# Kernel tuning notes

Hardware: AMD Instinct MI355X
Metric: run time of the kernel (lower is better)

The kernel has to match this reference:

```python
import jax, jax.numpy as jnp
import numpy as np

N = 8192      # nodes
D_IN = 128    # input features
D_H = 48      # GAT hidden (hardcoded in module)
D_OUT = 32    # control output dim
NEG_INF = -9e15  # matches torch code's -9000000000000000.0


def setup_inputs() -> dict:
    key = jax.random.key(0)
    ks = jax.random.split(key, 12)
    s = 0.05
    return {
        "x": jax.random.normal(ks[0], (N, D_IN), jnp.float32),
        "adj": jax.random.randint(ks[1], (N, N), 0, 2, jnp.int32),
        "W_gat": jax.random.normal(ks[2], (D_H, D_IN), jnp.float32) * s,
        "a": jax.random.normal(ks[3], (1, D_H), jnp.float32) * s,
        "gamma": jnp.ones((D_H,), jnp.float32),
        "beta": jnp.zeros((D_H,), jnp.float32),
        "W1": jax.random.normal(ks[4], (256, D_H), jnp.float32) * s,
        "b1": jnp.zeros((256,), jnp.float32),
        "W2": jax.random.normal(ks[5], (128, 256), jnp.float32) * s,
        "b2": jnp.zeros((128,), jnp.float32),
        "W3": jax.random.normal(ks[6], (D_OUT, 128), jnp.float32) * s,
        "b3": jnp.zeros((D_OUT,), jnp.float32),
    }


def reference(x, adj, W_gat, a, gamma, beta, W1, b1, W2, b2, W3, b3):
    # --- LightweightGATLayer ---
    Wh = x @ W_gat.T                      # [N, D_H]
    s = Wh @ a.T                          # [N, 1] additive attention scores
    e = s + s.T                           # [N, N]
    e = jnp.where(e > 0, e, 0.2 * e)      # LeakyReLU(0.2)
    e = jnp.where(adj > 0, e, NEG_INF)    # mask non-edges
    attn = jax.nn.softmax(e, axis=1)      # row softmax; dropout is identity in eval
    h_prime = attn @ Wh                   # [N, D_H]
    # LayerNorm over last dim, eps=1e-5
    mu = jnp.mean(h_prime, axis=-1, keepdims=True)
    var = jnp.var(h_prime, axis=-1, keepdims=True)
    h = (h_prime - mu) * jax.lax.rsqrt(var + 1e-5) * gamma + beta
    # --- BiACT MLP head: 48 -> 256 -> 128 -> D_OUT ---
    h = jax.nn.relu(h @ W1.T + b1)
    h = jax.nn.relu(h @ W2.T + b2)
    return h @ W3.T + b3                  # [N, D_OUT]
```

## Files before the change

kernel.cpp:

```cpp
#include <hip/hip_runtime.h>

#define N 8192
#define DIN 128
#define DH 48
#define MT 128
#define KC 64
#define PSTR 72
#define NSPLIT 16
#define JSPAN (N / NSPLIT)
#define NCHUNK (JSPAN / KC)
#define HSTR 49
#define RB 32

typedef _Float16 half8 __attribute__((ext_vector_type(8)));
typedef float f32x4 __attribute__((ext_vector_type(4)));

__global__ __launch_bounds__(256) void k_zero(float* __restrict__ hacc) {
    int i = blockIdx.x * 256 + threadIdx.x;
    if (i < N * HSTR) hacc[i] = 0.f;
}

__global__ __launch_bounds__(256) void k_wh(const float* __restrict__ x,
                                            const float* __restrict__ Wg,
                                            float* __restrict__ Wh) {
    __shared__ float wT[DIN * DH];
    int t = threadIdx.x;
    for (int e = t; e < DIN * DH; e += 256) {
        int c = e / DIN, k = e % DIN;
        wT[k * DH + c] = Wg[e];
    }
    __syncthreads();
    int o = blockIdx.x * 256 + t;
    int r = o / DH, c = o % DH;
    const float4* xr = (const float4*)(x + (size_t)r * DIN);
    float acc = 0.f;
    #pragma unroll 8
    for (int k4 = 0; k4 < DIN / 4; ++k4) {
        float4 xv = xr[k4];
        int kb = k4 * 4;
        acc += xv.x * wT[(kb + 0) * DH + c];
        acc += xv.y * wT[(kb + 1) * DH + c];
        acc += xv.z * wT[(kb + 2) * DH + c];
        acc += xv.w * wT[(kb + 3) * DH + c];
    }
    Wh[o] = acc;
}

__global__ __launch_bounds__(256) void k_s(const float* __restrict__ Wh,
                                           const float* __restrict__ a,
                                           float* __restrict__ s) {
    int r = blockIdx.x * 256 + threadIdx.x;
    const float4* wr = (const float4*)(Wh + (size_t)r * DH);
    const float4* av = (const float4*)a;
    float acc = 0.f;
    #pragma unroll
    for (int k4 = 0; k4 < DH / 4; ++k4) {
        float4 w = wr[k4]; float4 aa = av[k4];
        acc += w.x * aa.x + w.y * aa.y + w.z * aa.z + w.w * aa.w;
    }
    s[r] = acc;
}

__global__ __launch_bounds__(256) void k_tr(const float* __restrict__ Wh,
                                            _Float16* __restrict__ WhT) {
    __shared__ _Float16 tile[DH][72];
    int t = threadIdx.x;
    int r0 = blockIdx.x * 64;
    for (int e = t; e < 64 * DH; e += 256) {
        int r = e / DH, c = e % DH;
        tile[c][r] = (_Float16)Wh[(size_t)(r0 + r) * DH + c];
    }
    __syncthreads();
    for (int u = t; u < DH * 8; u += 256) {
        int c = u >> 3, g = u & 7;
        *(half8*)&WhT[(size_t)c * N + r0 + g * 8] = *(const half8*)&tile[c][g * 8];
    }
}

__global__ __launch_bounds__(256, 4) void k_gat(const int* __restrict__ adj,
                                                const _Float16* __restrict__ WhT,
                                                const float* __restrict__ s,
                                                float* __restrict__ hacc) {
    __shared__ _Float16 pS[MT][PSTR];
    __shared__ float sRow[MT];
    int t = threadIdx.x;
    int tile = blockIdx.x & 63;
    int split = blockIdx.x >> 6;
    int i0 = tile * MT;
    int jbase = split * JSPAN;

    if (t < MT) sRow[t] = s[i0 + t];

    int lane = t & 63, w = t >> 6;
    int ln16 = lane & 15, kq = lane >> 4;
    int jp = t & 31, rg = t >> 5;

    half8 bc;
    {
        _Float16 v = (ln16 == 0) ? (_Float16)1.0f : (_Float16)0.0f;
        #pragma unroll
        for (int i = 0; i < 8; ++i) bc[i] = v;
    }

    f32x4 acc[2][4];
    #pragma unroll
    for (int m = 0; m < 2; ++m)
        #pragma unroll
        for (int n = 0; n < 4; ++n) acc[m][n] = (f32x4){0.f, 0.f, 0.f, 0.f};

    __syncthreads();

    for (int chunk = 0; chunk < NCHUNK; ++chunk) {
        int j0 = jbase + chunk * KC;
        int2 av[16];
        {
            const int* abase = adj + (size_t)(i0 + rg * 16) * N + j0 + 2 * jp;
            #pragma unroll
            for (int it = 0; it < 16; ++it)
                av[it] = *(const int2*)(abase + (size_t)it * N);
        }
        half8 bfr[2][3];
        #pragma unroll
        for (int kt = 0; kt < 2; ++kt)
            #pragma unroll
            for (int nt = 0; nt < 3; ++nt)
                bfr[kt][nt] = *(const half8*)&WhT[(size_t)(nt * 16 + ln16) * N
                                                  + j0 + kt * 32 + kq * 8];
        {
            float2 sj = *(const float2*)(s + j0 + 2 * jp);
            #pragma unroll
            for (int it = 0; it < 16; ++it) {
                int r = rg * 16 + it;
                float e0 = sRow[r] + sj.x;
                float e1 = sRow[r] + sj.y;
                e0 = fmaxf(e0, 0.2f * e0);
                e1 = fmaxf(e1, 0.2f * e1);
                float p0 = av[it].x ? __expf(e0) : 0.f;
                float p1 = av[it].y ? __expf(e1) : 0.f;
                union { _Float16 h[2]; unsigned u; } pk;
                pk.h[0] = (_Float16)p0;
                pk.h[1] = (_Float16)p1;
                *(unsigned*)&pS[r][2 * jp] = pk.u;
            }
        }
        __syncthreads();
        {
            int m0 = w * 32;
            #pragma unroll
            for (int kt = 0; kt < 2; ++kt) {
                int kk = kt * 32 + kq * 8;
                #pragma unroll
                for (int mtl = 0; mtl < 2; ++mtl) {
                    half8 a = *(const half8*)&pS[m0 + mtl * 16 + ln16][kk];
                    acc[mtl][0] = __builtin_amdgcn_mfma_f32_16x16x32_f16(a, bfr[kt][0], acc[mtl][0], 0, 0, 0);
                    acc[mtl][1] = __builtin_amdgcn_mfma_f32_16x16x32_f16(a, bfr[kt][1], acc[mtl][1], 0, 0, 0);
                    acc[mtl][2] = __builtin_amdgcn_mfma_f32_16x16x32_f16(a, bfr[kt][2], acc[mtl][2], 0, 0, 0);
                    acc[mtl][3] = __builtin_amdgcn_mfma_f32_16x16x32_f16(a, bc,         acc[mtl][3], 0, 0, 0);
                }
            }
        }
        __syncthreads();
    }
    #pragma unroll
    for (int mtl = 0; mtl < 2; ++mtl) {
        int rbase = i0 + w * 32 + mtl * 16 + kq * 4;
        #pragma unroll
        for (int nt = 0; nt < 4; ++nt) {
            int col = nt * 16 + ln16;
            if (nt == 3 && ln16 != 0) continue;
            #pragma unroll
            for (int reg = 0; reg < 4; ++reg)
                atomicAdd(&hacc[(size_t)(rbase + reg) * HSTR + col], acc[mtl][nt][reg]);
        }
    }
}

__global__ __launch_bounds__(256) void k_mlp(const float* __restrict__ hacc,
                                             const float* __restrict__ gamma,
                                             const float* __restrict__ beta,
                                             const float* __restrict__ W1, const float* __restrict__ b1,
                                             const float* __restrict__ W2, const float* __restrict__ b2,
                                             const float* __restrict__ W3, const float* __restrict__ b3,
                                             float* __restrict__ out) {
    __shared__ float hs[RB * HSTR];
    __shared__ float hN[RB * DH];
    __shared__ float h1[RB * 256];
    __shared__ float h2[RB * 128];
    int t = threadIdx.x;
    int r0 = blockIdx.x * RB;

    for (int e = t; e < RB * HSTR; e += 256)
        hs[e] = hacc[(size_t)r0 * HSTR + e];
    __syncthreads();

    if (t < RB) {
        float invl = 1.f / hs[t * HSTR + 48];
        float sum = 0.f;
        for (int d = 0; d < DH; ++d) sum += hs[t * HSTR + d];
        float mean = sum * invl * (1.f / DH);
        float var = 0.f;
        for (int d = 0; d < DH; ++d) {
            float dv = hs[t * HSTR + d] * invl - mean;
            var += dv * dv;
        }
        var *= (1.f / DH);
        float rs = rsqrtf(var + 1e-5f);
        for (int d = 0; d < DH; ++d) {
            float hv = (hs[t * HSTR + d] * invl - mean) * rs;
            hN[t * DH + d] = hv * gamma[d] + beta[d];
        }
    }
    __syncthreads();

    {
        int c0 = (t & 127) * 2, c1 = c0 + 1;
        int rbeg = (t >> 7) * 16;
        float4 wa[12], wb[12];
        const float4* wr0 = (const float4*)(W1 + c0 * DH);
        const float4* wr1 = (const float4*)(W1 + c1 * DH);
        #pragma unroll
        for (int k4 = 0; k4 < 12; ++k4) { wa[k4] = wr0[k4]; wb[k4] = wr1[k4]; }
        float ba = b1[c0], bb = b1[c1];
        for (int r = rbeg; r < rbeg + 16; ++r) {
            const float4* hv4 = (const float4*)&hN[r * DH];
            float a0 = ba, a1 = bb;
            #pragma unroll
            for (int k4 = 0; k4 < 12; ++k4) {
                float4 hv = hv4[k4];
                a0 += hv.x * wa[k4].x + hv.y * wa[k4].y + hv.z * wa[k4].z + hv.w * wa[k4].w;
                a1 += hv.x * wb[k4].x + hv.y * wb[k4].y + hv.z * wb[k4].z + hv.w * wb[k4].w;
            }
            h1[r * 256 + c0] = fmaxf(a0, 0.f);
            h1[r * 256 + c1] = fmaxf(a1, 0.f);
        }
    }
    __syncthreads();

    {
        int c4 = (t & 31) * 4;
        int rr0 = (t >> 5) * 4;
        float a[4][4];
        #pragma unroll
        for (int rr = 0; rr < 4; ++rr)
            #pragma unroll
            for (int cc = 0; cc < 4; ++cc) a[rr][cc] = 0.f;
        for (int k4 = 0; k4 < 64; ++k4) {
            float4 h[4], wv[4];
            #pragma unroll
            for (int rr = 0; rr < 4; ++rr)
                h[rr] = *(const float4*)&h1[(rr0 + rr) * 256 + 4 * k4];
            #pragma unroll
            for (int cc = 0; cc < 4; ++cc)
                wv[cc] = *(const float4*)&W2[(size_t)(c4 + cc) * 256 + 4 * k4];
            #pragma unroll
            for (int rr = 0; rr < 4; ++rr)
                #pragma unroll
                for (int cc = 0; cc < 4; ++cc)
                    a[rr][cc] += h[rr].x * wv[cc].x + h[rr].y * wv[cc].y
                               + h[rr].z * wv[cc].z + h[rr].w * wv[cc].w;
        }
        #pragma unroll
        for (int rr = 0; rr < 4; ++rr)
            #pragma unroll
            for (int cc = 0; cc < 4; ++cc)
                h2[(rr0 + rr) * 128 + c4 + cc] = fmaxf(a[rr][cc] + b2[c4 + cc], 0.f);
    }
    __syncthreads();

    {
        int c = t & 31;
        int rr0 = (t >> 5) * 4;
        float a[4];
        float bias = b3[c];
        #pragma unroll
        for (int rr = 0; rr < 4; ++rr) a[rr] = bias;
        const float4* wrow = (const float4*)(W3 + c * 128);
        for (int k4 = 0; k4 < 32; ++k4) {
            float4 wv = wrow[k4];
            #pragma unroll
            for (int rr = 0; rr < 4; ++rr) {
                float4 hv = *(const float4*)&h2[(rr0 + rr) * 128 + 4 * k4];
                a[rr] += wv.x * hv.x + wv.y * hv.y + wv.z * hv.z + wv.w * hv.w;
            }
        }
        #pragma unroll
        for (int rr = 0; rr < 4; ++rr)
            out[(size_t)(r0 + rr0 + rr) * 32 + c] = a[rr];
    }
}

extern "C" void kernel_launch(void* const* d_in, const int* in_sizes, int n_in,
                              void* d_out, int out_size, void* d_ws, size_t ws_size,
                              hipStream_t stream) {
    const float* x     = (const float*)d_in[0];
    const int*   adj   = (const int*)d_in[1];
    const float* Wg    = (const float*)d_in[2];
    const float* a     = (const float*)d_in[3];
    const float* gamma = (const float*)d_in[4];
    const float* beta  = (const float*)d_in[5];
    const float* W1    = (const float*)d_in[6];
    const float* b1    = (const float*)d_in[7];
    const float* W2    = (const float*)d_in[8];
    const float* b2    = (const float*)d_in[9];
    const float* W3    = (const float*)d_in[10];
    const float* b3    = (const float*)d_in[11];
    float* out = (float*)d_out;

    float* ws = (float*)d_ws;
    float*     Wh   = ws;
    float*     s    = ws + (size_t)N * DH;
    _Float16*  WhT  = (_Float16*)(ws + (size_t)N * DH + N);
    float*     hacc = ws + (size_t)N * DH + N + (size_t)N * DH / 2;

    k_zero<<<(N * HSTR + 255) / 256, 256, 0, stream>>>(hacc);
    k_wh<<<N * DH / 256, 256, 0, stream>>>(x, Wg, Wh);
    k_s<<<N / 256, 256, 0, stream>>>(Wh, a, s);
    k_tr<<<N / 64, 256, 0, stream>>>(Wh, WhT);
    k_gat<<<64 * NSPLIT, 256, 0, stream>>>(adj, WhT, s, hacc);
    k_mlp<<<N / RB, 256, 0, stream>>>(hacc, gamma, beta, W1, b1, W2, b2, W3, b3, out);
}
```

Measured before the change: 497.6 us.

## Double-buffer GAT chunks with register prefetch and replace atomics with split partial sums

The GAT kernel now prefetches the next chunk's adjacency values into registers and stages the transposed Wh tile through double-buffered shared memory. This is meant to overlap global loads with the exp and MFMA work and to drop one barrier per chunk. The atomicAdd reduction into a zeroed accumulator is replaced by per-split partial stores, which the MLP kernel sums; that removes the zero kernel and the atomic contention. In exchange it uses more LDS and registers (launch bounds lowered to 3 waves) and adds a 16-way reduction read of a larger workspace.

```diff
diff --git a/kernel.cpp b/kernel.cpp
--- a/kernel.cpp
+++ b/kernel.cpp
@@ -9,16 +9,12 @@
 #define NSPLIT 16
 #define JSPAN (N / NSPLIT)
 #define NCHUNK (JSPAN / KC)
+#define ACC_STRIDE 64
 #define HSTR 49
 #define RB 32
 
 typedef _Float16 half8 __attribute__((ext_vector_type(8)));
 typedef float f32x4 __attribute__((ext_vector_type(4)));
-
-__global__ __launch_bounds__(256) void k_zero(float* __restrict__ hacc) {
-    int i = blockIdx.x * 256 + threadIdx.x;
-    if (i < N * HSTR) hacc[i] = 0.f;
-}
 
 __global__ __launch_bounds__(256) void k_wh(const float* __restrict__ x,
                                             const float* __restrict__ Wg,
@@ -77,11 +73,12 @@
     }
 }
 
-__global__ __launch_bounds__(256, 4) void k_gat(const int* __restrict__ adj,
+__global__ __launch_bounds__(256, 3) void k_gat(const int* __restrict__ adj,
                                                 const _Float16* __restrict__ WhT,
                                                 const float* __restrict__ s,
-                                                float* __restrict__ hacc) {
-    __shared__ _Float16 pS[MT][PSTR];
+                                                float* __restrict__ accWs) {
+    __shared__ _Float16 pS[2][MT][PSTR];
+    __shared__ _Float16 wS[2][DH][PSTR];
     __shared__ float sRow[MT];
     int t = threadIdx.x;
     int tile = blockIdx.x & 63;
@@ -108,24 +105,39 @@
         #pragma unroll
         for (int n = 0; n < 4; ++n) acc[m][n] = (f32x4){0.f, 0.f, 0.f, 0.f};
 
-    __syncthreads();
-
+    const int* arow = adj + (size_t)(i0 + rg * 16) * N + 2 * jp;
+
+    int2 av[16];
+    #pragma unroll
+    for (int it = 0; it < 16; ++it)
+        av[it] = *(const int2*)(arow + (size_t)it * N + jbase);
+    {
+        int u0 = t;
+        int row = u0 >> 3, s8 = u0 & 3 ;
+        s8 = u0 & 7;
+        if (u0 < 384) {  }
+        half8 v0 = *(const half8*)&WhT[(size_t)row * N + jbase + s8 * 8];
+        *(half8*)&wS[0][row][s8 * 8] = v0;
+        if (t < 128) {
+            int u1 = 256 + t;
+            int row1 = u1 >> 3, s81 = u1 & 7;
+            half8 v1 = *(const half8*)&WhT[(size_t)row1 * N + jbase + s81 * 8];
+            *(half8*)&wS[0][row1][s81 * 8] = v1;
+        }
+    }
+    __syncthreads();
+
+    int buf = 0;
     for (int chunk = 0; chunk < NCHUNK; ++chunk) {
         int j0 = jbase + chunk * KC;
-        int2 av[16];
-        {
-            const int* abase = adj + (size_t)(i0 + rg * 16) * N + j0 + 2 * jp;
+        bool more = (chunk + 1 < NCHUNK);
+        int2 avn[16];
+        if (more) {
+            const int* ab = arow + (j0 + KC);
             #pragma unroll
             for (int it = 0; it < 16; ++it)
-                av[it] = *(const int2*)(abase + (size_t)it * N);
-        }
-        half8 bfr[2][3];
-        #pragma unroll
-        for (int kt = 0; kt < 2; ++kt)
-            #pragma unroll
-            for (int nt = 0; nt < 3; ++nt)
-                bfr[kt][nt] = *(const half8*)&WhT[(size_t)(nt * 16 + ln16) * N
-                                                  + j0 + kt * 32 + kq * 8];
+                avn[it] = *(const int2*)(ab + (size_t)it * N);
+        }
         {
             float2 sj = *(const float2*)(s + j0 + 2 * jp);
             #pragma unroll
@@ -140,42 +152,61 @@
                 union { _Float16 h[2]; unsigned u; } pk;
                 pk.h[0] = (_Float16)p0;
                 pk.h[1] = (_Float16)p1;
-                *(unsigned*)&pS[r][2 * jp] = pk.u;
+                *(unsigned*)&pS[buf][r][2 * jp] = pk.u;
             }
         }
         __syncthreads();
+        half8 wv0, wv1;
+        int row0 = t >> 3, s80 = t & 7;
+        int row1 = (256 + t) >> 3, s81 = t & 7;
+        if (more) {
+            int jn = j0 + KC;
+            wv0 = *(const half8*)&WhT[(size_t)row0 * N + jn + s80 * 8];
+            if (t < 128)
+                wv1 = *(const half8*)&WhT[(size_t)row1 * N + jn + s81 * 8];
+        }
         {
             int m0 = w * 32;
             #pragma unroll
             for (int kt = 0; kt < 2; ++kt) {
                 int kk = kt * 32 + kq * 8;
+                half8 b0 = *(const half8*)&wS[buf][0 + ln16][kk];
+                half8 b1 = *(const half8*)&wS[buf][16 + ln16][kk];
+                half8 b2 = *(const half8*)&wS[buf][32 + ln16][kk];
                 #pragma unroll
                 for (int mtl = 0; mtl < 2; ++mtl) {
-                    half8 a = *(const half8*)&pS[m0 + mtl * 16 + ln16][kk];
-                    acc[mtl][0] = __builtin_amdgcn_mfma_f32_16x16x32_f16(a, bfr[kt][0], acc[mtl][0], 0, 0, 0);
-                    acc[mtl][1] = __builtin_amdgcn_mfma_f32_16x16x32_f16(a, bfr[kt][1], acc[mtl][1], 0, 0, 0);
-                    acc[mtl][2] = __builtin_amdgcn_mfma_f32_16x16x32_f16(a, bfr[kt][2], acc[mtl][2], 0, 0, 0);
-                    acc[mtl][3] = __builtin_amdgcn_mfma_f32_16x16x32_f16(a, bc,         acc[mtl][3], 0, 0, 0);
+                    half8 a = *(const half8*)&pS[buf][m0 + mtl * 16 + ln16][kk];
+                    acc[mtl][0] = __builtin_amdgcn_mfma_f32_16x16x32_f16(a, b0, acc[mtl][0], 0, 0, 0);
+                    acc[mtl][1] = __builtin_amdgcn_mfma_f32_16x16x32_f16(a, b1, acc[mtl][1], 0, 0, 0);
+                    acc[mtl][2] = __builtin_amdgcn_mfma_f32_16x16x32_f16(a, b2, acc[mtl][2], 0, 0, 0);
+                    acc[mtl][3] = __builtin_amdgcn_mfma_f32_16x16x32_f16(a, bc, acc[mtl][3], 0, 0, 0);
                 }
             }
         }
-        __syncthreads();
+        if (more) {
+            *(half8*)&wS[buf ^ 1][row0][s80 * 8] = wv0;
+            if (t < 128)
+                *(half8*)&wS[buf ^ 1][row1][s81 * 8] = wv1;
+        }
+        #pragma unroll
+        for (int it = 0; it < 16; ++it) av[it] = avn[it];
+        buf ^= 1;
     }
     #pragma unroll
     for (int mtl = 0; mtl < 2; ++mtl) {
-        int rbase = i0 + w * 32 + mtl * 16 + kq * 4;
+        size_t rbase = (size_t)split * N + i0 + w * 32 + mtl * 16 + kq * 4;
         #pragma unroll
         for (int nt = 0; nt < 4; ++nt) {
             int col = nt * 16 + ln16;
             if (nt == 3 && ln16 != 0) continue;
             #pragma unroll
             for (int reg = 0; reg < 4; ++reg)
-                atomicAdd(&hacc[(size_t)(rbase + reg) * HSTR + col], acc[mtl][nt][reg]);
-        }
-    }
-}
-
-__global__ __launch_bounds__(256) void k_mlp(const float* __restrict__ hacc,
+                accWs[(rbase + reg) * ACC_STRIDE + col] = acc[mtl][nt][reg];
+        }
+    }
+}
+
+__global__ __launch_bounds__(256) void k_mlp(const float* __restrict__ accWs,
                                              const float* __restrict__ gamma,
                                              const float* __restrict__ beta,
                                              const float* __restrict__ W1, const float* __restrict__ b1,
@@ -189,8 +220,15 @@
     int t = threadIdx.x;
     int r0 = blockIdx.x * RB;
 
-    for (int e = t; e < RB * HSTR; e += 256)
-        hs[e] = hacc[(size_t)r0 * HSTR + e];
+    for (int e = t; e < RB * HSTR; e += 256) {
+        int r = e / HSTR, d = e % HSTR;
+        size_t base = (size_t)(r0 + r) * ACC_STRIDE + d;
+        float v = 0.f;
+        #pragma unroll
+        for (int sp = 0; sp < NSPLIT; ++sp)
+            v += accWs[(size_t)sp * N * ACC_STRIDE + base];
+        hs[e] = v;
+    }
     __syncthreads();
 
     if (t < RB) {
@@ -307,15 +345,14 @@
     float* out = (float*)d_out;
 
     float* ws = (float*)d_ws;
-    float*     Wh   = ws;
-    float*     s    = ws + (size_t)N * DH;
-    _Float16*  WhT  = (_Float16*)(ws + (size_t)N * DH + N);
-    float*     hacc = ws + (size_t)N * DH + N + (size_t)N * DH / 2;
-
-    k_zero<<<(N * HSTR + 255) / 256, 256, 0, stream>>>(hacc);
+    float*     Wh    = ws;
+    float*     s     = ws + (size_t)N * DH;
+    _Float16*  WhT   = (_Float16*)(ws + (size_t)N * DH + N);
+    float*     accWs = ws + (size_t)N * DH + N + (size_t)N * DH / 2;
+
     k_wh<<<N * DH / 256, 256, 0, stream>>>(x, Wg, Wh);
     k_s<<<N / 256, 256, 0, stream>>>(Wh, a, s);
     k_tr<<<N / 64, 256, 0, stream>>>(Wh, WhT);
-    k_gat<<<64 * NSPLIT, 256, 0, stream>>>(adj, WhT, s, hacc);
-    k_mlp<<<N / RB, 256, 0, stream>>>(hacc, gamma, beta, W1, b1, W2, b2, W3, b3, out);
-}
+    k_gat<<<64 * NSPLIT, 256, 0, stream>>>(adj, WhT, s, accWs);
+    k_mlp<<<N / RB, 256, 0, stream>>>(accWs, gamma, beta, W1, b1, W2, b2, W3, b3, out);
+}
```

New measurement: 481.7 us. 1.03x faster.

## Build attention probabilities directly in MFMA A-fragments and replace atomics with split partials

Applied to the files above, without the earlier changes.

Each lane now loads its own adjacency and score values matching the MFMA A-operand layout and computes the exp-masked probabilities in registers. This removes the shared-memory staging of P and both block barriers per chunk. The atomic accumulation into a zeroed buffer becomes plain stores of per-split partial sums, which the MLP kernel reduces, so the zero kernel is dropped. The cost is a 16x larger partial buffer read in k_mlp, and adjacency loads that are now strided per lane rather than coalesced by row.

```diff
diff --git a/kernel.cpp b/kernel.cpp
--- a/kernel.cpp
+++ b/kernel.cpp
@@ -5,20 +5,15 @@
 #define DH 48
 #define MT 128
 #define KC 64
-#define PSTR 72
 #define NSPLIT 16
 #define JSPAN (N / NSPLIT)
 #define NCHUNK (JSPAN / KC)
+#define ACC_STRIDE 64
 #define HSTR 49
 #define RB 32
 
 typedef _Float16 half8 __attribute__((ext_vector_type(8)));
 typedef float f32x4 __attribute__((ext_vector_type(4)));
-
-__global__ __launch_bounds__(256) void k_zero(float* __restrict__ hacc) {
-    int i = blockIdx.x * 256 + threadIdx.x;
-    if (i < N * HSTR) hacc[i] = 0.f;
-}
 
 __global__ __launch_bounds__(256) void k_wh(const float* __restrict__ x,
                                             const float* __restrict__ Wg,
@@ -77,23 +72,37 @@
     }
 }
 
+__device__ inline half8 mk_p(float si, float4 sa, float4 sb, int4 m0, int4 m1) {
+    float e0 = si + sa.x, e1 = si + sa.y, e2 = si + sa.z, e3 = si + sa.w;
+    float e4 = si + sb.x, e5 = si + sb.y, e6 = si + sb.z, e7 = si + sb.w;
+    e0 = fmaxf(e0, 0.2f * e0); e1 = fmaxf(e1, 0.2f * e1);
+    e2 = fmaxf(e2, 0.2f * e2); e3 = fmaxf(e3, 0.2f * e3);
+    e4 = fmaxf(e4, 0.2f * e4); e5 = fmaxf(e5, 0.2f * e5);
+    e6 = fmaxf(e6, 0.2f * e6); e7 = fmaxf(e7, 0.2f * e7);
+    half8 r;
+    r[0] = (_Float16)(m0.x ? __expf(e0) : 0.f);
+    r[1] = (_Float16)(m0.y ? __expf(e1) : 0.f);
+    r[2] = (_Float16)(m0.z ? __expf(e2) : 0.f);
+    r[3] = (_Float16)(m0.w ? __expf(e3) : 0.f);
+    r[4] = (_Float16)(m1.x ? __expf(e4) : 0.f);
+    r[5] = (_Float16)(m1.y ? __expf(e5) : 0.f);
+    r[6] = (_Float16)(m1.z ? __expf(e6) : 0.f);
+    r[7] = (_Float16)(m1.w ? __expf(e7) : 0.f);
+    return r;
+}
+
 __global__ __launch_bounds__(256, 4) void k_gat(const int* __restrict__ adj,
                                                 const _Float16* __restrict__ WhT,
                                                 const float* __restrict__ s,
-                                                float* __restrict__ hacc) {
-    __shared__ _Float16 pS[MT][PSTR];
-    __shared__ float sRow[MT];
+                                                float* __restrict__ accWs) {
     int t = threadIdx.x;
     int tile = blockIdx.x & 63;
     int split = blockIdx.x >> 6;
     int i0 = tile * MT;
     int jbase = split * JSPAN;
 
-    if (t < MT) sRow[t] = s[i0 + t];
-
     int lane = t & 63, w = t >> 6;
     int ln16 = lane & 15, kq = lane >> 4;
-    int jp = t & 31, rg = t >> 5;
 
     half8 bc;
     {
@@ -108,74 +117,75 @@
         #pragma unroll
         for (int n = 0; n < 4; ++n) acc[m][n] = (f32x4){0.f, 0.f, 0.f, 0.f};
 
-    __syncthreads();
+    const int row0 = i0 + w * 32 + ln16;
+    const int row1 = row0 + 16;
+    const float si0 = s[row0];
+    const float si1 = s[row1];
+    const int* ar0 = adj + (size_t)row0 * N;
+    const int* ar1 = adj + (size_t)row1 * N;
 
     for (int chunk = 0; chunk < NCHUNK; ++chunk) {
-        int j0 = jbase + chunk * KC;
-        int2 av[16];
-        {
-            const int* abase = adj + (size_t)(i0 + rg * 16) * N + j0 + 2 * jp;
-            #pragma unroll
-            for (int it = 0; it < 16; ++it)
-                av[it] = *(const int2*)(abase + (size_t)it * N);
-        }
-        half8 bfr[2][3];
-        #pragma unroll
-        for (int kt = 0; kt < 2; ++kt)
-            #pragma unroll
-            for (int nt = 0; nt < 3; ++nt)
-                bfr[kt][nt] = *(const half8*)&WhT[(size_t)(nt * 16 + ln16) * N
-                                                  + j0 + kt * 32 + kq * 8];
-        {
-            float2 sj = *(const float2*)(s + j0 + 2 * jp);
-            #pragma unroll
-            for (int it = 0; it < 16; ++it) {
-                int r = rg * 16 + it;
-                float e0 = sRow[r] + sj.x;
-                float e1 = sRow[r] + sj.y;
-                e0 = fmaxf(e0, 0.2f * e0);
-                e1 = fmaxf(e1, 0.2f * e1);
-                float p0 = av[it].x ? __expf(e0) : 0.f;
-                float p1 = av[it].y ? __expf(e1) : 0.f;
-                union { _Float16 h[2]; unsigned u; } pk;
-                pk.h[0] = (_Float16)p0;
-                pk.h[1] = (_Float16)p1;
-                *(unsigned*)&pS[r][2 * jp] = pk.u;
-            }
-        }
-        __syncthreads();
-        {
-            int m0 = w * 32;
-            #pragma unroll
-            for (int kt = 0; kt < 2; ++kt) {
-                int kk = kt * 32 + kq * 8;
-                #pragma unroll
-                for (int mtl = 0; mtl < 2; ++mtl) {
-                    half8 a = *(const half8*)&pS[m0 + mtl * 16 + ln16][kk];
-                    acc[mtl][0] = __builtin_amdgcn_mfma_f32_16x16x32_f16(a, bfr[kt][0], acc[mtl][0], 0, 0, 0);
-                    acc[mtl][1] = __builtin_amdgcn_mfma_f32_16x16x32_f16(a, bfr[kt][1], acc[mtl][1], 0, 0, 0);
-                    acc[mtl][2] = __builtin_amdgcn_mfma_f32_16x16x32_f16(a, bfr[kt][2], acc[mtl][2], 0, 0, 0);
-                    acc[mtl][3] = __builtin_amdgcn_mfma_f32_16x16x32_f16(a, bc,         acc[mtl][3], 0, 0, 0);
-                }
-            }
-        }
-        __syncthreads();
-    }
+        const int j0 = jbase + chunk * KC;
+        const int jk0 = j0 + kq * 8;
+        const int jk1 = jk0 + 32;
+
+        int4 m00a = *(const int4*)(ar0 + jk0);
+        int4 m00b = *(const int4*)(ar0 + jk0 + 4);
+        int4 m01a = *(const int4*)(ar0 + jk1);
+        int4 m01b = *(const int4*)(ar0 + jk1 + 4);
+        int4 m10a = *(const int4*)(ar1 + jk0);
+        int4 m10b = *(const int4*)(ar1 + jk0 + 4);
+        int4 m11a = *(const int4*)(ar1 + jk1);
+        int4 m11b = *(const int4*)(ar1 + jk1 + 4);
+        float4 s0a = *(const float4*)(s + jk0);
+        float4 s0b = *(const float4*)(s + jk0 + 4);
+        float4 s1a = *(const float4*)(s + jk1);
+        float4 s1b = *(const float4*)(s + jk1 + 4);
+        half8 bf00 = *(const half8*)&WhT[(size_t)(0  + ln16) * N + jk0];
+        half8 bf01 = *(const half8*)&WhT[(size_t)(16 + ln16) * N + jk0];
+        half8 bf02 = *(const half8*)&WhT[(size_t)(32 + ln16) * N + jk0];
+        half8 bf10 = *(const half8*)&WhT[(size_t)(0  + ln16) * N + jk1];
+        half8 bf11 = *(const half8*)&WhT[(size_t)(16 + ln16) * N + jk1];
+        half8 bf12 = *(const half8*)&WhT[(size_t)(32 + ln16) * N + jk1];
+
+        half8 a00 = mk_p(si0, s0a, s0b, m00a, m00b);
+        half8 a01 = mk_p(si0, s1a, s1b, m01a, m01b);
+        half8 a10 = mk_p(si1, s0a, s0b, m10a, m10b);
+        half8 a11 = mk_p(si1, s1a, s1b, m11a, m11b);
+
+        acc[0][0] = __builtin_amdgcn_mfma_f32_16x16x32_f16(a00, bf00, acc[0][0], 0, 0, 0);
+        acc[0][1] = __builtin_amdgcn_mfma_f32_16x16x32_f16(a00, bf01, acc[0][1], 0, 0, 0);
+        acc[0][2] = __builtin_amdgcn_mfma_f32_16x16x32_f16(a00, bf02, acc[0][2], 0, 0, 0);
+        acc[0][3] = __builtin_amdgcn_mfma_f32_16x16x32_f16(a00, bc,   acc[0][3], 0, 0, 0);
+        acc[1][0] = __builtin_amdgcn_mfma_f32_16x16x32_f16(a10, bf00, acc[1][0], 0, 0, 0);
+        acc[1][1] = __builtin_amdgcn_mfma_f32_16x16x32_f16(a10, bf01, acc[1][1], 0, 0, 0);
+        acc[1][2] = __builtin_amdgcn_mfma_f32_16x16x32_f16(a10, bf02, acc[1][2], 0, 0, 0);
+        acc[1][3] = __builtin_amdgcn_mfma_f32_16x16x32_f16(a10, bc,   acc[1][3], 0, 0, 0);
+        acc[0][0] = __builtin_amdgcn_mfma_f32_16x16x32_f16(a01, bf10, acc[0][0], 0, 0, 0);
+        acc[0][1] = __builtin_amdgcn_mfma_f32_16x16x32_f16(a01, bf11, acc[0][1], 0, 0, 0);
+        acc[0][2] = __builtin_amdgcn_mfma_f32_16x16x32_f16(a01, bf12, acc[0][2], 0, 0, 0);
+        acc[0][3] = __builtin_amdgcn_mfma_f32_16x16x32_f16(a01, bc,   acc[0][3], 0, 0, 0);
+        acc[1][0] = __builtin_amdgcn_mfma_f32_16x16x32_f16(a11, bf10, acc[1][0], 0, 0, 0);
+        acc[1][1] = __builtin_amdgcn_mfma_f32_16x16x32_f16(a11, bf11, acc[1][1], 0, 0, 0);
+        acc[1][2] = __builtin_amdgcn_mfma_f32_16x16x32_f16(a11, bf12, acc[1][2], 0, 0, 0);
+        acc[1][3] = __builtin_amdgcn_mfma_f32_16x16x32_f16(a11, bc,   acc[1][3], 0, 0, 0);
+    }
+
     #pragma unroll
     for (int mtl = 0; mtl < 2; ++mtl) {
-        int rbase = i0 + w * 32 + mtl * 16 + kq * 4;
+        size_t rbase = (size_t)split * N + i0 + w * 32 + mtl * 16 + kq * 4;
         #pragma unroll
         for (int nt = 0; nt < 4; ++nt) {
             int col = nt * 16 + ln16;
             if (nt == 3 && ln16 != 0) continue;
             #pragma unroll
             for (int reg = 0; reg < 4; ++reg)
-                atomicAdd(&hacc[(size_t)(rbase + reg) * HSTR + col], acc[mtl][nt][reg]);
-        }
-    }
-}
-
-__global__ __launch_bounds__(256) void k_mlp(const float* __restrict__ hacc,
+                accWs[(rbase + reg) * ACC_STRIDE + col] = acc[mtl][nt][reg];
+        }
+    }
+}
+
+__global__ __launch_bounds__(256) void k_mlp(const float* __restrict__ accWs,
                                              const float* __restrict__ gamma,
                                              const float* __restrict__ beta,
                                              const float* __restrict__ W1, const float* __restrict__ b1,
@@ -189,8 +199,15 @@
     int t = threadIdx.x;
     int r0 = blockIdx.x * RB;
 
-    for (int e = t; e < RB * HSTR; e += 256)
-        hs[e] = hacc[(size_t)r0 * HSTR + e];
+    for (int e = t; e < RB * HSTR; e += 256) {
+        int r = e / HSTR, d = e % HSTR;
+        size_t base = (size_t)(r0 + r) * ACC_STRIDE + d;
+        float v = 0.f;
+        #pragma unroll
+        for (int sp = 0; sp < NSPLIT; ++sp)
+            v += accWs[(size_t)sp * N * ACC_STRIDE + base];
+        hs[e] = v;
+    }
     __syncthreads();
 
     if (t < RB) {
@@ -307,15 +324,14 @@
     float* out = (float*)d_out;
 
     float* ws = (float*)d_ws;
-    float*     Wh   = ws;
-    float*     s    = ws + (size_t)N * DH;
-    _Float16*  WhT  = (_Float16*)(ws + (size_t)N * DH + N);
-    float*     hacc = ws + (size_t)N * DH + N + (size_t)N * DH / 2;
-
-    k_zero<<<(N * HSTR + 255) / 256, 256, 0, stream>>>(hacc);
+    float*     Wh    = ws;
+    float*     s     = ws + (size_t)N * DH;
+    _Float16*  WhT   = (_Float16*)(ws + (size_t)N * DH + N);
+    float*     accWs = ws + (size_t)N * DH + N + (size_t)N * DH / 2;
+
     k_wh<<<N * DH / 256, 256, 0, stream>>>(x, Wg, Wh);
     k_s<<<N / 256, 256, 0, stream>>>(Wh, a, s);
     k_tr<<<N / 64, 256, 0, stream>>>(Wh, WhT);
-    k_gat<<<64 * NSPLIT, 256, 0, stream>>>(adj, WhT, s, hacc);
-    k_mlp<<<N / RB, 256, 0, stream>>>(hacc, gamma, beta, W1, b1, W2, b2, W3, b3, out);
-}
+    k_gat<<<64 * NSPLIT, 256, 0, stream>>>(adj, WhT, s, accWs);
+    k_mlp<<<N / RB, 256, 0, stream>>>(accWs, gamma, beta, W1, b1, W2, b2, W3, b3, out);
+}
```

Result: faster. 480.6 us (-3.4%).
